# Optimization experiments

Hardware: AMD Instinct MI355X
Metric: run time of the kernel (lower is better)

The kernel has to match this reference:

```python
import jax, jax.numpy as jnp
import numpy as np

DEPTH = 5  # hyperdimensional_depth default


def _hyper_layer(x, hw, cw, cb):
    """Faithful vectorized HyperdimensionalNeuralLayer.forward.

    x: [B, D_in], hw: [DEPTH, D_in, D_out], cw: [D_in, D_out], cb: [D_out].
    The torch code loops over batch i and output dim j; the state is
    independent of i and of x, so we only vmap over j (via leading axis)
    and scan over depth. For D_in > 2 the hand-built rotation matrix is
    cos*I - sin*S + sin*S^T with S the +1 circular shift.
    """
    d_in, d_out = cw.shape
    classical = x @ cw + cb  # [B, D_out]
    angles = hw[:, :d_out, 0]  # [DEPTH, D_out] (torch indexes hw[depth, j, 0])
    phases = hw[:, :d_out, 1]  # [DEPTH, D_out]
    s0 = jnp.full((d_out, d_in), 1.0 / np.sqrt(d_in), dtype=jnp.complex64)

    def step(s, ap):
        a, p = ap  # each [D_out]
        c = jnp.cos(a)[:, None]
        sn = jnp.sin(a)[:, None]
        # (R @ s)[k] = cos*s[k] - sin*s[k+1] + sin*s[k-1] (circular)
        s = c * s - sn * jnp.roll(s, -1, axis=1) + sn * jnp.roll(s, 1, axis=1)
        s = s * jnp.exp(1j * p)[:, None]  # phase gate: scalar complex mult
        return s, None

    sT, _ = jax.lax.scan(step, s0, (angles, phases))
    prob = jnp.abs(sT[:, 0]) ** 2  # [D_out], real
    return jnp.tanh(classical + prob[None, :].astype(classical.dtype))


def setup_inputs() -> dict:
    key = jax.random.key(0)
    ks = jax.random.split(key, 16)
    B, IN, H, OUT = 8192, 1024, 2048, 1024
    f = jnp.float32
    return {
        "x": jax.random.normal(ks[0], (B, IN), f),
        "w0": jax.random.normal(ks[1], (IN, H), f) * 0.02,
        "b0": jax.random.normal(ks[2], (H,), f) * 0.02,
        "w1": jax.random.normal(ks[3], (H, H), f) * 0.02,
        "b1": jax.random.normal(ks[4], (H,), f) * 0.02,
        "hw0": jax.random.normal(ks[5], (DEPTH, H, H), f),
        "cw0": jax.random.normal(ks[6], (H, H), f) * 0.02,
        "cb0": jax.random.normal(ks[7], (H,), f) * 0.02,
        "w2": jax.random.normal(ks[8], (H, H), f) * 0.02,
        "b2": jax.random.normal(ks[9], (H,), f) * 0.02,
        "hw1": jax.random.normal(ks[10], (DEPTH, H, H), f),
        "cw1": jax.random.normal(ks[11], (H, H), f) * 0.02,
        "cb1": jax.random.normal(ks[12], (H,), f) * 0.02,
        "wf": jax.random.normal(ks[13], (H, OUT), f) * 0.02,
        "bf": jax.random.normal(ks[14], (OUT,), f) * 0.02,
    }


def reference(x, w0, b0, w1, b1, hw0, cw0, cb0, w2, b2, hw1, cw1, cb1, wf, bf):
    # Linear layers get relu; hyper layers apply tanh internally (per torch forward)
    h = jax.nn.relu(x @ w0 + b0)
    h = jax.nn.relu(h @ w1 + b1)
    h = _hyper_layer(h, hw0, cw0, cb0)
    h = jax.nn.relu(h @ w2 + b2)
    h = _hyper_layer(h, hw1, cw1, cb1)
    return jax.nn.relu(h @ wf + bf)
```

## Files before the change

kernel.cpp:

```cpp
#include <hip/hip_runtime.h>
#include <math.h>


typedef __attribute__((ext_vector_type(8))) __bf16 bfrag;
typedef __attribute__((ext_vector_type(4))) float f32x4;

__device__ __forceinline__ void gload_lds16(const void* g, void* l) {
  __builtin_amdgcn_global_load_lds(
      (__attribute__((address_space(1))) void*)g,
      (__attribute__((address_space(3))) void*)l, 16, 0, 0);
}

__device__ __forceinline__ f32x4 mfma16(bfrag a, bfrag b, f32x4 c) {
  return __builtin_amdgcn_mfma_f32_16x16x32_bf16(a, b, c, 0, 0, 0);
}

template <int EPI>
__global__ __launch_bounds__(256) void hnn_gemm(
    const __bf16* __restrict__ A, const __bf16* __restrict__ Bt,
    const float* __restrict__ bias, __bf16* __restrict__ outAct,
    float* __restrict__ outF32, int M, int N, int K) {
  __shared__ __align__(1024) __bf16 As[128 * 64];
  __shared__ __align__(1024) __bf16 Bs[128 * 64];

  const int tid = threadIdx.x;
  const int lane = tid & 63;
  const int wid = tid >> 6;
  const int wr = wid >> 1, wc = wid & 1;
  const int lr = lane & 15, kg = lane >> 4;
  const int swz = (lr & 7) << 4;

  const size_t ldA = (size_t)K;
  const size_t ldB = 2 * (size_t)K;
  const __bf16* gA = A + (size_t)(blockIdx.y * 128) * ldA;
  const __bf16* gB = Bt + (size_t)(blockIdx.x * 128) * ldB;

  const bool isA = (wid < 2);
  const __bf16* gsrc = isA ? gA : gB;
  const size_t lds = isA ? ldA : ldB;
  __bf16* lbase = isA ? As : Bs;
  const int cbase = (wid & 1) * 8;
  const int srow = lane >> 3;
  const int sblk = lane & 7;
  const int lblk = sblk ^ srow;

  f32x4 acc[4][4] = {};

  const int KT = K / 64;
  int seg = 0, ko = 0;
  for (int it = 0; it < 2 * KT; ++it) {
    const int kW = seg * K + ko;
    const int kt = isA ? ko : kW;

#pragma unroll
    for (int i = 0; i < 8; ++i) {
      const int c = cbase + i;
      const int row = c * 8 + srow;
      gload_lds16(gsrc + (size_t)row * lds + (size_t)(kt + lblk * 8),
                  lbase + c * 512);
    }
    __syncthreads();

#pragma unroll
    for (int ks = 0; ks < 2; ++ks) {
      bfrag a[4], b[4];
      const int cb2 = (ks * 64 + kg * 16) ^ swz;
#pragma unroll
      for (int m = 0; m < 4; ++m) {
        const int row = wr * 64 + m * 16 + lr;
        a[m] = *(const bfrag*)((const char*)As + row * 128 + cb2);
      }
#pragma unroll
      for (int n = 0; n < 4; ++n) {
        const int row = wc * 64 + n * 16 + lr;
        b[n] = *(const bfrag*)((const char*)Bs + row * 128 + cb2);
      }
#pragma unroll
      for (int m = 0; m < 4; ++m)
#pragma unroll
        for (int n = 0; n < 4; ++n) acc[m][n] = mfma16(a[m], b[n], acc[m][n]);
    }
    __syncthreads();

    ko += 64;
    if (ko == K) { ko = 0; ++seg; }
  }

  const int rowBase = blockIdx.y * 128 + wr * 64;
  const int colBase = blockIdx.x * 128 + wc * 64;
#pragma unroll
  for (int n = 0; n < 4; ++n) {
    const int col = colBase + n * 16 + lr;
    const float bv = bias[col];
#pragma unroll
    for (int m = 0; m < 4; ++m) {
      const int row0 = rowBase + m * 16 + kg * 4;
#pragma unroll
      for (int r = 0; r < 4; ++r) {
        float v = acc[m][n][r] + bv;
        if (EPI == 1)
          v = tanhf(v);
        else
          v = fmaxf(v, 0.0f);
        const int row = row0 + r;
        if (EPI == 2) {
          outF32[(size_t)row * N + col] = v;
        } else {
          outAct[(size_t)row * N + col] = (__bf16)v;
        }
      }
    }
  }
}

__global__ __launch_bounds__(256) void xconv(const float* __restrict__ x,
                                             __bf16* __restrict__ out) {
  const size_t idx = (size_t)blockIdx.x * 256 + threadIdx.x;
  out[idx] = (__bf16)x[idx];
}

__global__ __launch_bounds__(256) void wconv(const float* __restrict__ W,
                                             __bf16* __restrict__ Wt, int K,
                                             int N) {
  __shared__ float tile[32][33];
  const int tx = threadIdx.x, ty = threadIdx.y;
  const int n0 = blockIdx.x * 32, k0 = blockIdx.y * 32;
#pragma unroll
  for (int i = 0; i < 32; i += 8)
    tile[ty + i][tx] = W[(size_t)(k0 + ty + i) * N + n0 + tx];
  __syncthreads();
#pragma unroll
  for (int i = 0; i < 32; i += 8) {
    const int n = n0 + ty + i;
    const int k = k0 + tx;
    const float v = tile[tx][ty + i];
    const __bf16 hi = (__bf16)v;
    const float lo = v - (float)hi;
    __bf16* o = Wt + (size_t)n * (2 * (size_t)K) + k;
    o[0] = hi;
    o[K] = (__bf16)lo;
  }
}

__global__ __launch_bounds__(256) void probk(const float* __restrict__ hw,
                                             const float* __restrict__ cb,
                                             float* __restrict__ pbias, int H) {
  const int j = blockIdx.x * 256 + threadIdx.x;
  if (j >= H) return;
  float p = 1.0f / (float)H;
#pragma unroll
  for (int t = 0; t < 5; ++t) {
    const float a = hw[(size_t)t * H * H + (size_t)j * H];
    const float c = cosf(a);
    p *= c * c;
  }
  pbias[j] = cb[j] + p;
}

extern "C" void kernel_launch(void* const* d_in, const int* in_sizes, int n_in,
                              void* d_out, int out_size, void* d_ws,
                              size_t ws_size, hipStream_t stream) {
  (void)in_sizes;
  (void)n_in;
  (void)out_size;
  (void)ws_size;
  const float* x = (const float*)d_in[0];
  const float* w0 = (const float*)d_in[1];
  const float* b0 = (const float*)d_in[2];
  const float* w1 = (const float*)d_in[3];
  const float* b1 = (const float*)d_in[4];
  const float* hw0 = (const float*)d_in[5];
  const float* cw0 = (const float*)d_in[6];
  const float* cb0 = (const float*)d_in[7];
  const float* w2 = (const float*)d_in[8];
  const float* b2 = (const float*)d_in[9];
  const float* hw1 = (const float*)d_in[10];
  const float* cw1 = (const float*)d_in[11];
  const float* cb1 = (const float*)d_in[12];
  const float* wf = (const float*)d_in[13];
  const float* bf = (const float*)d_in[14];

  char* ws = (char*)d_ws;
  __bf16* actA = (__bf16*)ws;
  __bf16* actB = (__bf16*)(ws + ((size_t)64 << 20));
  char* p = ws + ((size_t)128 << 20);
  __bf16* wt0 = (__bf16*)p;  p += (size_t)2048 * 2048 * 2;
  __bf16* wt1 = (__bf16*)p;  p += (size_t)2048 * 4096 * 2;
  __bf16* wtc0 = (__bf16*)p; p += (size_t)2048 * 4096 * 2;
  __bf16* wt2 = (__bf16*)p;  p += (size_t)2048 * 4096 * 2;
  __bf16* wtc1 = (__bf16*)p; p += (size_t)2048 * 4096 * 2;
  __bf16* wtf = (__bf16*)p;  p += (size_t)1024 * 4096 * 2;
  float* pb0 = (float*)p;    p += 2048 * 4;
  float* pb1 = (float*)p;    p += 2048 * 4;

  xconv<<<(8192 * 1024) / 256, 256, 0, stream>>>(x, actA);
  wconv<<<dim3(2048 / 32, 1024 / 32), dim3(32, 8), 0, stream>>>(w0, wt0, 1024,
                                                                2048);
  wconv<<<dim3(2048 / 32, 2048 / 32), dim3(32, 8), 0, stream>>>(w1, wt1, 2048,
                                                                2048);
  wconv<<<dim3(2048 / 32, 2048 / 32), dim3(32, 8), 0, stream>>>(cw0, wtc0,
                                                                2048, 2048);
  wconv<<<dim3(2048 / 32, 2048 / 32), dim3(32, 8), 0, stream>>>(w2, wt2, 2048,
                                                                2048);
  wconv<<<dim3(2048 / 32, 2048 / 32), dim3(32, 8), 0, stream>>>(cw1, wtc1,
                                                                2048, 2048);
  wconv<<<dim3(1024 / 32, 2048 / 32), dim3(32, 8), 0, stream>>>(wf, wtf, 2048,
                                                                1024);
  probk<<<8, 256, 0, stream>>>(hw0, cb0, pb0, 2048);
  probk<<<8, 256, 0, stream>>>(hw1, cb1, pb1, 2048);

  hnn_gemm<0><<<dim3(16, 64), 256, 0, stream>>>(actA, wt0, b0, actB, nullptr,
                                                8192, 2048, 1024);
  hnn_gemm<0><<<dim3(16, 64), 256, 0, stream>>>(actB, wt1, b1, actA, nullptr,
                                                8192, 2048, 2048);
  hnn_gemm<1><<<dim3(16, 64), 256, 0, stream>>>(actA, wtc0, pb0, actB, nullptr,
                                                8192, 2048, 2048);
  hnn_gemm<0><<<dim3(16, 64), 256, 0, stream>>>(actB, wt2, b2, actA, nullptr,
                                                8192, 2048, 2048);
  hnn_gemm<1><<<dim3(16, 64), 256, 0, stream>>>(actA, wtc1, pb1, actB, nullptr,
                                                8192, 2048, 2048);
  hnn_gemm<2><<<dim3(8, 64), 256, 0, stream>>>(actB, wtf, bf, nullptr,
                                               (float*)d_out, 8192, 1024, 2048);
}
```

Measured before the change: 1.112 ms.

## Rewrite GEMM as 256x256 tile with double-buffered LDS and interleaved loads

The bf16 GEMM moves from a 128x128 tile with 4 waves and a single LDS buffer to a 256x256 tile with 8 waves and 128KB of double-buffered LDS. Global-to-LDS loads for the next K step are split into four chunks and issued between four MFMA phases, with s_setprio raising priority during compute. Blocks are remapped across 8 XCD groups to improve L2 locality. The goal is to hide memory latency and raise arithmetic intensity per load. The cost is heavier register and LDS pressure, and the declared 2 blocks per CU may not fit with 128KB of LDS per block.

Result: faster. 912.7 us (-17.9%).

```diff
diff --git a/kernel.cpp b/kernel.cpp
--- a/kernel.cpp
+++ b/kernel.cpp
@@ -16,84 +16,161 @@
 }
 
 template <int EPI>
-__global__ __launch_bounds__(256) void hnn_gemm(
+__global__ __launch_bounds__(512, 2) void hnn_gemm(
     const __bf16* __restrict__ A, const __bf16* __restrict__ Bt,
     const float* __restrict__ bias, __bf16* __restrict__ outAct,
     float* __restrict__ outF32, int M, int N, int K) {
-  __shared__ __align__(1024) __bf16 As[128 * 64];
-  __shared__ __align__(1024) __bf16 Bs[128 * 64];
+  __shared__ __align__(1024) char smem[131072];
 
   const int tid = threadIdx.x;
   const int lane = tid & 63;
   const int wid = tid >> 6;
-  const int wr = wid >> 1, wc = wid & 1;
+  const int wr = wid >> 2;
+  const int wc = wid & 3;
   const int lr = lane & 15, kg = lane >> 4;
   const int swz = (lr & 7) << 4;
+  const int c0 = (kg * 16) ^ swz;
+  const int c1 = (64 + kg * 16) ^ swz;
+
+  const int nwg = gridDim.x * gridDim.y;
+  const int bid = blockIdx.y * gridDim.x + blockIdx.x;
+  const int cpx = nwg >> 3;
+  const int sid = (bid & 7) * cpx + (bid >> 3);
+  const int bx = sid % gridDim.x;
+  const int by = sid / gridDim.x;
 
   const size_t ldA = (size_t)K;
   const size_t ldB = 2 * (size_t)K;
-  const __bf16* gA = A + (size_t)(blockIdx.y * 128) * ldA;
-  const __bf16* gB = Bt + (size_t)(blockIdx.x * 128) * ldB;
-
-  const bool isA = (wid < 2);
-  const __bf16* gsrc = isA ? gA : gB;
-  const size_t lds = isA ? ldA : ldB;
-  __bf16* lbase = isA ? As : Bs;
-  const int cbase = (wid & 1) * 8;
-  const int srow = lane >> 3;
-  const int sblk = lane & 7;
-  const int lblk = sblk ^ srow;
-
-  f32x4 acc[4][4] = {};
-
-  const int KT = K / 64;
-  int seg = 0, ko = 0;
-  for (int it = 0; it < 2 * KT; ++it) {
-    const int kW = seg * K + ko;
-    const int kt = isA ? ko : kW;
-
-#pragma unroll
-    for (int i = 0; i < 8; ++i) {
-      const int c = cbase + i;
-      const int row = c * 8 + srow;
-      gload_lds16(gsrc + (size_t)row * lds + (size_t)(kt + lblk * 8),
-                  lbase + c * 512);
-    }
+
+  const int srow = tid >> 3;
+  const int lblk = (tid & 7) ^ (srow & 7);
+  const __bf16* pA = A + ((size_t)(by * 256 + srow)) * ldA + lblk * 8;
+  const __bf16* pB = Bt + ((size_t)(bx * 256 + srow)) * ldB + lblk * 8;
+  const int dst0 = tid * 16;
+
+  f32x4 acc[8][4] = {};
+
+  const int KT2 = (2 * K) >> 6;
+
+  {
+    char* Ad = smem;
+    char* Bd = smem + 32768;
+    gload_lds16(pA, Ad + dst0);
+    gload_lds16(pA + 64 * ldA, Ad + dst0 + 8192);
+    gload_lds16(pA + 128 * ldA, Ad + 16384 + dst0);
+    gload_lds16(pA + 192 * ldA, Ad + 16384 + dst0 + 8192);
+    gload_lds16(pB, Bd + dst0);
+    gload_lds16(pB + 64 * ldB, Bd + dst0 + 8192);
+    gload_lds16(pB + 128 * ldB, Bd + 16384 + dst0);
+    gload_lds16(pB + 192 * ldB, Bd + 16384 + dst0 + 8192);
+  }
+  __syncthreads();
+
+  const int arow = wr * 128 + lr;
+  const int brow = wc * 64 + lr;
+
+  for (int t = 0; t < KT2; ++t) {
+    const int cur = t & 1;
+    const char* Ab = smem + cur * 65536;
+    const char* Bb = Ab + 32768;
+    char* Adn = smem + (cur ^ 1) * 65536;
+    char* Bdn = Adn + 32768;
+    const int tn = (t + 1 < KT2) ? t + 1 : t;
+    const int kAn = (tn << 6) & (K - 1);
+    const int kBn = tn << 6;
+
+    bfrag am[4][2], bn0[2][2], bn1[2][2];
+
+#pragma unroll
+    for (int mi = 0; mi < 4; ++mi) {
+      const int r = arow + mi * 16;
+      am[mi][0] = *(const bfrag*)(Ab + r * 128 + c0);
+      am[mi][1] = *(const bfrag*)(Ab + r * 128 + c1);
+    }
+#pragma unroll
+    for (int ni = 0; ni < 2; ++ni) {
+      const int r = brow + ni * 16;
+      bn0[ni][0] = *(const bfrag*)(Bb + r * 128 + c0);
+      bn0[ni][1] = *(const bfrag*)(Bb + r * 128 + c1);
+    }
+    gload_lds16(pA + kAn, Adn + dst0);
+    gload_lds16(pA + 64 * ldA + kAn, Adn + dst0 + 8192);
+    __builtin_amdgcn_s_barrier();
+    __builtin_amdgcn_s_setprio(1);
+#pragma unroll
+    for (int ks = 0; ks < 2; ++ks)
+#pragma unroll
+      for (int mi = 0; mi < 4; ++mi)
+#pragma unroll
+        for (int ni = 0; ni < 2; ++ni)
+          acc[mi][ni] = mfma16(am[mi][ks], bn0[ni][ks], acc[mi][ni]);
+    __builtin_amdgcn_s_setprio(0);
+    __builtin_amdgcn_s_barrier();
+
+#pragma unroll
+    for (int ni = 0; ni < 2; ++ni) {
+      const int r = brow + (2 + ni) * 16;
+      bn1[ni][0] = *(const bfrag*)(Bb + r * 128 + c0);
+      bn1[ni][1] = *(const bfrag*)(Bb + r * 128 + c1);
+    }
+    gload_lds16(pA + 128 * ldA + kAn, Adn + 16384 + dst0);
+    gload_lds16(pA + 192 * ldA + kAn, Adn + 16384 + dst0 + 8192);
+    __builtin_amdgcn_s_barrier();
+    __builtin_amdgcn_s_setprio(1);
+#pragma unroll
+    for (int ks = 0; ks < 2; ++ks)
+#pragma unroll
+      for (int mi = 0; mi < 4; ++mi)
+#pragma unroll
+        for (int ni = 0; ni < 2; ++ni)
+          acc[mi][2 + ni] = mfma16(am[mi][ks], bn1[ni][ks], acc[mi][2 + ni]);
+    __builtin_amdgcn_s_setprio(0);
+    __builtin_amdgcn_s_barrier();
+
+#pragma unroll
+    for (int mi = 0; mi < 4; ++mi) {
+      const int r = arow + (4 + mi) * 16;
+      am[mi][0] = *(const bfrag*)(Ab + r * 128 + c0);
+      am[mi][1] = *(const bfrag*)(Ab + r * 128 + c1);
+    }
+    gload_lds16(pB + kBn, Bdn + dst0);
+    gload_lds16(pB + 64 * ldB + kBn, Bdn + dst0 + 8192);
+    __builtin_amdgcn_s_barrier();
+    __builtin_amdgcn_s_setprio(1);
+#pragma unroll
+    for (int ks = 0; ks < 2; ++ks)
+#pragma unroll
+      for (int mi = 0; mi < 4; ++mi)
+#pragma unroll
+        for (int ni = 0; ni < 2; ++ni)
+          acc[4 + mi][2 + ni] =
+              mfma16(am[mi][ks], bn1[ni][ks], acc[4 + mi][2 + ni]);
+    __builtin_amdgcn_s_setprio(0);
+    __builtin_amdgcn_s_barrier();
+
+    gload_lds16(pB + 128 * ldB + kBn, Bdn + 16384 + dst0);
+    gload_lds16(pB + 192 * ldB + kBn, Bdn + 16384 + dst0 + 8192);
+    __builtin_amdgcn_s_barrier();
+    __builtin_amdgcn_s_setprio(1);
+#pragma unroll
+    for (int ks = 0; ks < 2; ++ks)
+#pragma unroll
+      for (int mi = 0; mi < 4; ++mi)
+#pragma unroll
+        for (int ni = 0; ni < 2; ++ni)
+          acc[4 + mi][ni] = mfma16(am[mi][ks], bn0[ni][ks], acc[4 + mi][ni]);
+    __builtin_amdgcn_s_setprio(0);
     __syncthreads();
-
-#pragma unroll
-    for (int ks = 0; ks < 2; ++ks) {
-      bfrag a[4], b[4];
-      const int cb2 = (ks * 64 + kg * 16) ^ swz;
-#pragma unroll
-      for (int m = 0; m < 4; ++m) {
-        const int row = wr * 64 + m * 16 + lr;
-        a[m] = *(const bfrag*)((const char*)As + row * 128 + cb2);
-      }
-#pragma unroll
-      for (int n = 0; n < 4; ++n) {
-        const int row = wc * 64 + n * 16 + lr;
-        b[n] = *(const bfrag*)((const char*)Bs + row * 128 + cb2);
-      }
-#pragma unroll
-      for (int m = 0; m < 4; ++m)
-#pragma unroll
-        for (int n = 0; n < 4; ++n) acc[m][n] = mfma16(a[m], b[n], acc[m][n]);
-    }
-    __syncthreads();
-
-    ko += 64;
-    if (ko == K) { ko = 0; ++seg; }
-  }
-
-  const int rowBase = blockIdx.y * 128 + wr * 64;
-  const int colBase = blockIdx.x * 128 + wc * 64;
+  }
+
+  const int rowBase = by * 256 + wr * 128;
+  const int colBase = bx * 256 + wc * 64;
 #pragma unroll
   for (int n = 0; n < 4; ++n) {
     const int col = colBase + n * 16 + lr;
     const float bv = bias[col];
 #pragma unroll
-    for (int m = 0; m < 4; ++m) {
+    for (int m = 0; m < 8; ++m) {
       const int row0 = rowBase + m * 16 + kg * 4;
 #pragma unroll
       for (int r = 0; r < 4; ++r) {
@@ -209,16 +286,16 @@
   probk<<<8, 256, 0, stream>>>(hw0, cb0, pb0, 2048);
   probk<<<8, 256, 0, stream>>>(hw1, cb1, pb1, 2048);
 
-  hnn_gemm<0><<<dim3(16, 64), 256, 0, stream>>>(actA, wt0, b0, actB, nullptr,
-                                                8192, 2048, 1024);
-  hnn_gemm<0><<<dim3(16, 64), 256, 0, stream>>>(actB, wt1, b1, actA, nullptr,
-                                                8192, 2048, 2048);
-  hnn_gemm<1><<<dim3(16, 64), 256, 0, stream>>>(actA, wtc0, pb0, actB, nullptr,
-                                                8192, 2048, 2048);
-  hnn_gemm<0><<<dim3(16, 64), 256, 0, stream>>>(actB, wt2, b2, actA, nullptr,
-                                                8192, 2048, 2048);
-  hnn_gemm<1><<<dim3(16, 64), 256, 0, stream>>>(actA, wtc1, pb1, actB, nullptr,
-                                                8192, 2048, 2048);
-  hnn_gemm<2><<<dim3(8, 64), 256, 0, stream>>>(actB, wtf, bf, nullptr,
+  hnn_gemm<0><<<dim3(8, 32), 512, 0, stream>>>(actA, wt0, b0, actB, nullptr,
+                                               8192, 2048, 1024);
+  hnn_gemm<0><<<dim3(8, 32), 512, 0, stream>>>(actB, wt1, b1, actA, nullptr,
+                                               8192, 2048, 2048);
+  hnn_gemm<1><<<dim3(8, 32), 512, 0, stream>>>(actA, wtc0, pb0, actB, nullptr,
+                                               8192, 2048, 2048);
+  hnn_gemm<0><<<dim3(8, 32), 512, 0, stream>>>(actB, wt2, b2, actA, nullptr,
+                                               8192, 2048, 2048);
+  hnn_gemm<1><<<dim3(8, 32), 512, 0, stream>>>(actA, wtc1, pb1, actB, nullptr,
+                                               8192, 2048, 2048);
+  hnn_gemm<2><<<dim3(4, 32), 512, 0, stream>>>(actB, wtf, bf, nullptr,
                                                (float*)d_out, 8192, 1024, 2048);
 }
```
